# Optimization experiments

Hardware: AMD Instinct MI355X
Metric: run time of the kernel (lower is better)

The kernel has to match this reference:

```python
import jax, jax.numpy as jnp
import numpy as np

N_TX, N_USER, N_MERCH = 100000, 20000, 5000
E = 400000
F_IN, H, L = 32, 256, 2


def setup_inputs() -> dict:
    key = jax.random.key(0)
    ks = jax.random.split(key, 24)
    p = lambda k, s: 0.02 * jax.random.normal(k, s, dtype=jnp.float32)
    return {
        "x_tx": jax.random.normal(ks[0], (N_TX, F_IN), dtype=jnp.float32),
        "x_user": jax.random.normal(ks[1], (N_USER, H), dtype=jnp.float32),
        "x_merch": jax.random.normal(ks[2], (N_MERCH, H), dtype=jnp.float32),
        # input projection
        "Wp": p(ks[3], (F_IN, H)), "bp": jnp.zeros((H,), jnp.float32),
        # per-layer, per-edge-type SAGEConv params: lin_l (neighbor, with bias) and lin_r (root, no bias)
        "Wl": p(ks[4], (L, 4, H, H)), "bl": jnp.zeros((L, 4, H), jnp.float32),
        "Wr": p(ks[5], (L, 4, H, H)),
        # classifier head
        "Wc1": p(ks[6], (H, H // 2)), "bc1": jnp.zeros((H // 2,), jnp.float32),
        "Wc2": p(ks[7], (H // 2, 1)), "bc2": jnp.zeros((1,), jnp.float32),
        # revenue head
        "Wv1": p(ks[8], (H, H // 2)), "bv1": jnp.zeros((H // 2,), jnp.float32),
        "Wv2": p(ks[9], (H // 2, 1)), "bv2": jnp.zeros((1,), jnp.float32),
        # edge lists (src, dst) per relation
        "e_ut_src": jax.random.randint(ks[10], (E,), 0, N_USER, dtype=jnp.int32),
        "e_ut_dst": jax.random.randint(ks[11], (E,), 0, N_TX, dtype=jnp.int32),
        "e_tm_src": jax.random.randint(ks[12], (E,), 0, N_TX, dtype=jnp.int32),
        "e_tm_dst": jax.random.randint(ks[13], (E,), 0, N_MERCH, dtype=jnp.int32),
        "e_mt_src": jax.random.randint(ks[14], (E,), 0, N_MERCH, dtype=jnp.int32),
        "e_mt_dst": jax.random.randint(ks[15], (E,), 0, N_TX, dtype=jnp.int32),
        "e_tu_src": jax.random.randint(ks[16], (E,), 0, N_TX, dtype=jnp.int32),
        "e_tu_dst": jax.random.randint(ks[17], (E,), 0, N_USER, dtype=jnp.int32),
    }


def _seg_mean(x_src, src, dst, n_dst):
    # gather source features per edge, scatter-mean into destinations
    msg = x_src[src]                                        # [E, H]
    s = jax.ops.segment_sum(msg, dst, num_segments=n_dst)   # [n_dst, H]
    cnt = jax.ops.segment_sum(jnp.ones((dst.shape[0],), x_src.dtype), dst, num_segments=n_dst)
    return s / jnp.maximum(cnt, 1.0)[:, None]


def _sage(x_src, x_dst, src, dst, Wl, bl, Wr):
    # PyG SAGEConv: lin_l(mean_neighbors) + lin_r(x_dst)
    m = _seg_mean(x_src, src, dst, x_dst.shape[0])
    return m @ Wl + bl + x_dst @ Wr


def reference(x_tx, x_user, x_merch, Wp, bp, Wl, bl, Wr,
              Wc1, bc1, Wc2, bc2, Wv1, bv1, Wv2, bv2,
              e_ut_src, e_ut_dst, e_tm_src, e_tm_dst,
              e_mt_src, e_mt_dst, e_tu_src, e_tu_dst):
    xt = x_tx @ Wp + bp          # input_proj on 'transaction'
    xu, xm = x_user, x_merch     # already hidden_dim -> used as-is
    for l in range(L):
        t_from_u = _sage(xu, xt, e_ut_src, e_ut_dst, Wl[l, 0], bl[l, 0], Wr[l, 0])
        m_from_t = _sage(xt, xm, e_tm_src, e_tm_dst, Wl[l, 1], bl[l, 1], Wr[l, 1])
        t_from_m = _sage(xm, xt, e_mt_src, e_mt_dst, Wl[l, 2], bl[l, 2], Wr[l, 2])
        u_from_t = _sage(xt, xu, e_tu_src, e_tu_dst, Wl[l, 3], bl[l, 3], Wr[l, 3])
        # HeteroConv aggr='mean' over edge types per destination, then ReLU (dropout = identity in eval)
        xt = jax.nn.relu(0.5 * (t_from_u + t_from_m))
        xm = jax.nn.relu(m_from_t)
        xu = jax.nn.relu(u_from_t)
    fraud_logits = (jax.nn.relu(xt @ Wc1 + bc1) @ Wc2 + bc2)[:, 0]
    revenue_pred = (jax.nn.relu(xt @ Wv1 + bv1) @ Wv2 + bv2)[:, 0]
    return fraud_logits, revenue_pred
```

## Files before the change

kernel.cpp:

```cpp
#include <hip/hip_runtime.h>

#define NTX 100000
#define NUSER 20000
#define NMERCH 5000
#define HD 256
#define ROWPAD 128

using u16 = unsigned short;
typedef __attribute__((ext_vector_type(8))) short bf16x8;
typedef __attribute__((ext_vector_type(4))) float f32x4;

__device__ __forceinline__ u16 f2bf(float f){
  unsigned u = __float_as_uint(f);
  unsigned r = (u + 0x7FFFu + ((u >> 16) & 1u)) >> 16;
  return (u16)r;
}
__device__ __forceinline__ float bf2f(u16 b){
  return __uint_as_float(((unsigned)b) << 16);
}
__device__ __forceinline__ unsigned pk2(float a, float b){
  return (unsigned)f2bf(a) | ((unsigned)f2bf(b) << 16);
}

__device__ __forceinline__ void gather4(const u16* __restrict__ T, const int* __restrict__ ss,
    int j0, int j1, int lane, int c, float& o0, float& o1, float& o2, float& o3){
  float a0=0,a1=0,a2=0,a3=0, b0=0,b1=0,b2=0,b3=0;
  float c0=0,c1=0,c2=0,c3=0, d0=0,d1=0,d2=0,d3=0;
  for (int base = j0; base < j1; base += 64){
    int n = j1 - base; if (n > 64) n = 64;
    int idx = ss[base + (lane < n ? lane : 0)];
    for (int jj = 0; jj < n; jj += 4){
      int s0 = __shfl(idx, jj);
      int s1 = __shfl(idx, jj+1);
      int s2 = __shfl(idx, jj+2);
      int s3 = __shfl(idx, jj+3);
      ushort4 v0 = *(const ushort4*)(T + (size_t)s0*HD + c);
      ushort4 v1 = *(const ushort4*)(T + (size_t)s1*HD + c);
      ushort4 v2 = *(const ushort4*)(T + (size_t)s2*HD + c);
      ushort4 v3 = *(const ushort4*)(T + (size_t)s3*HD + c);
      a0 += bf2f(v0.x); a1 += bf2f(v0.y); a2 += bf2f(v0.z); a3 += bf2f(v0.w);
      if (jj+1 < n){ b0 += bf2f(v1.x); b1 += bf2f(v1.y); b2 += bf2f(v1.z); b3 += bf2f(v1.w); }
      if (jj+2 < n){ c0 += bf2f(v2.x); c1 += bf2f(v2.y); c2 += bf2f(v2.z); c3 += bf2f(v2.w); }
      if (jj+3 < n){ d0 += bf2f(v3.x); d1 += bf2f(v3.y); d2 += bf2f(v3.z); d3 += bf2f(v3.w); }
    }
  }
  o0 += (a0+b0)+(c0+d0); o1 += (a1+b1)+(c1+d1);
  o2 += (a2+b2)+(c2+d2); o3 += (a3+b3)+(c3+d3);
}

__device__ __forceinline__ int rel_n(int y){ return y==0?NTX: y==1?NMERCH: y==2?NTX:NUSER; }
__device__ __forceinline__ int rel_coff(int y){ return y==0?0: y==1?100000: y==2?105000:205000; }
__device__ __forceinline__ int rel_rpoff(int y){ return y==0?0: y==1?100001: y==2?105002:205003; }
__device__ __forceinline__ int rel_shift(int y){ return y==0?11: y==1?8: y==2?11:10; }
__device__ __forceinline__ int rel_np(int y){ return y==0?49: y==1?20: y==2?49:20; }
#define ECH 128
#define PSTW 72

__global__ __launch_bounds__(256) void csrA_kernel(const int* __restrict__ d0p, const int* __restrict__ d1p,
    const int* __restrict__ d2p, const int* __restrict__ d3p, int nE, int* __restrict__ PC){
  int y = blockIdx.y;
  const int* dst = y==0?d0p: y==1?d1p: y==2?d2p:d3p;
  int shift = rel_shift(y);
  __shared__ int cc[64];
  int t = threadIdx.x;
  if (t < 64) cc[t] = 0;
  __syncthreads();
  int CH = (nE + ECH - 1)/ECH;
  int e0 = blockIdx.x*CH, e1 = e0 + CH; if (e1 > nE) e1 = nE;
  for (int e = e0 + t*4; e < e1; e += 1024){
    int a = dst[e];
    int b = (e+1 < e1) ? dst[e+1] : -1;
    int c = (e+2 < e1) ? dst[e+2] : -1;
    int d = (e+3 < e1) ? dst[e+3] : -1;
    atomicAdd(&cc[a>>shift], 1);
    if (b >= 0) atomicAdd(&cc[b>>shift], 1);
    if (c >= 0) atomicAdd(&cc[c>>shift], 1);
    if (d >= 0) atomicAdd(&cc[d>>shift], 1);
  }
  __syncthreads();
  if (t < 64) PC[(((size_t)y*ECH + blockIdx.x)<<6) + t] = cc[t];
}

__global__ void csrB_kernel(int* __restrict__ PC, int* __restrict__ PST, int* __restrict__ RP, int nE){
  int y = blockIdx.y;
  int np = rel_np(y);
  int t = threadIdx.x;
  __shared__ int sh[64];
  int run = 0;
  if (t < np){
    for (int c = 0; c < ECH; ++c){
      size_t idx = (((size_t)y*ECH + c)<<6) + t;
      int v = PC[idx]; PC[idx] = run; run += v;
    }
  }
  sh[t] = run;
  __syncthreads();
  if (t == 0){
    int acc = 0;
    for (int i = 0; i < np; ++i){ int v = sh[i]; sh[i] = acc; acc += v; }
    PST[y*PSTW + np] = nE;
    RP[rel_rpoff(y) + rel_n(y)] = nE;
  }
  __syncthreads();
  if (t < np){
    int base = sh[t];
    PST[y*PSTW + t] = base;
    for (int c = 0; c < ECH; ++c){
      size_t idx = (((size_t)y*ECH + c)<<6) + t;
      PC[idx] += base;
    }
  }
}

__global__ __launch_bounds__(256) void csrC_kernel(
    const int* __restrict__ s0p, const int* __restrict__ d0p,
    const int* __restrict__ s1p, const int* __restrict__ d1p,
    const int* __restrict__ s2p, const int* __restrict__ d2p,
    const int* __restrict__ s3p, const int* __restrict__ d3p,
    const int* __restrict__ PC, int* __restrict__ EB, int nE){
  int y = blockIdx.y;
  const int* src = y==0?s0p: y==1?s1p: y==2?s2p:s3p;
  const int* dst = y==0?d0p: y==1?d1p: y==2?d2p:d3p;
  int shift = rel_shift(y);
  int mask = (1<<shift) - 1;
  __shared__ int cur[64];
  int t = threadIdx.x;
  if (t < 64) cur[t] = PC[(((size_t)y*ECH + blockIdx.x)<<6) + t];
  __syncthreads();
  int CH = (nE + ECH - 1)/ECH;
  int e0 = blockIdx.x*CH, e1 = e0 + CH; if (e1 > nE) e1 = nE;
  int* eb = EB + (size_t)y*nE;
  for (int e = e0 + t*4; e < e1; e += 1024){
    #pragma unroll
    for (int u = 0; u < 4; ++u){
      int ee = e + u;
      if (ee < e1){
        int d = dst[ee], s = src[ee];
        int pos = atomicAdd(&cur[d>>shift], 1);
        eb[pos] = ((d & mask) << 17) | s;
      }
    }
  }
}

__global__ __launch_bounds__(256) void csrD_kernel(const int* __restrict__ EB, const int* __restrict__ PST,
    int* __restrict__ RP, float* __restrict__ INV,
    int* __restrict__ ss0, int* __restrict__ ss1, int* __restrict__ ss2, int* __restrict__ ss3, int nE){
  int y = blockIdx.y;
  int np = rel_np(y);
  int part = blockIdx.x;
  if (part >= np) return;
  int shift = rel_shift(y);
  int n = rel_n(y);
  int gbase = part << shift;
  int len = n - gbase; int range = 1 << shift; if (len > range) len = range;
  __shared__ int cnt[2048];
  __shared__ int curs[2048];
  __shared__ int sh[256];
  int t = threadIdx.x;
  for (int i = t; i < len; i += 256) cnt[i] = 0;
  __syncthreads();
  const int* eb = EB + (size_t)y*nE;
  int j0 = PST[y*PSTW + part], j1 = PST[y*PSTW + part + 1];
  for (int j = j0 + t*4; j < j1; j += 1024){
    int a = eb[j];
    int b = (j+1 < j1) ? eb[j+1] : -1;
    int c = (j+2 < j1) ? eb[j+2] : -1;
    int d = (j+3 < j1) ? eb[j+3] : -1;
    atomicAdd(&cnt[a>>17], 1);
    if (b >= 0) atomicAdd(&cnt[b>>17], 1);
    if (c >= 0) atomicAdd(&cnt[c>>17], 1);
    if (d >= 0) atomicAdd(&cnt[d>>17], 1);
  }
  __syncthreads();
  int base8 = t*8;
  int vals[8]; int tsum = 0;
  #pragma unroll
  for (int u = 0; u < 8; ++u){
    int i = base8 + u;
    int v = (i < len) ? cnt[i] : 0;
    vals[u] = tsum; tsum += v;
  }
  sh[t] = tsum;
  __syncthreads();
  for (int o = 1; o < 256; o <<= 1){
    int v = (t >= o) ? sh[t-o] : 0;
    __syncthreads();
    sh[t] += v;
    __syncthreads();
  }
  int tbase = j0 + sh[t] - tsum;
  int rpo = rel_rpoff(y) + gbase;
  int ivo = rel_coff(y) + gbase;
  #pragma unroll
  for (int u = 0; u < 8; ++u){
    int i = base8 + u;
    if (i < len){
      int start = tbase + vals[u];
      curs[i] = start;
      RP[rpo + i] = start;
      INV[ivo + i] = 1.f/fmaxf((float)cnt[i], 1.f);
    }
  }
  __syncthreads();
  int* ss = y==0?ss0: y==1?ss1: y==2?ss2:ss3;
  for (int j = j0 + t*4; j < j1; j += 1024){
    #pragma unroll
    for (int u = 0; u < 4; ++u){
      int jj = j + u;
      if (jj < j1){
        int pk = eb[jj];
        int pos = atomicAdd(&curs[pk>>17], 1);
        ss[pos] = pk & 0x1FFFF;
      }
    }
  }
}

__global__ __launch_bounds__(256) void wprep_kernel(const float* __restrict__ Wl, const float* __restrict__ Wr,
    const float* __restrict__ Wp, const float* __restrict__ Wc1, const float* __restrict__ Wv1,
    const float* __restrict__ bc1, const float* __restrict__ bv1,
    u16* __restrict__ WTl, u16* __restrict__ WTr1, u16* __restrict__ WTr3, u16* __restrict__ WT02,
    u16* __restrict__ WTH, u16* __restrict__ WTp, float* __restrict__ bH){
  int y = blockIdx.y;
  int i = blockIdx.x*256 + threadIdx.x;
  if (y < 8){
    if (i < 65536){ int k=i>>8, n=i&255; WTl[(size_t)y*65536 + n*256 + k] = f2bf(Wl[(size_t)y*65536 + i]); }
  } else if (y < 10){
    int l = y-8;
    if (i < 65536){ int k=i>>8, n=i&255; WTr1[(size_t)l*65536 + n*256 + k] = f2bf(Wr[(size_t)(l*4+1)*65536 + i]); }
  } else if (y < 12){
    int l = y-10;
    if (i < 65536){ int k=i>>8, n=i&255; WTr3[(size_t)l*65536 + n*256 + k] = f2bf(Wr[(size_t)(l*4+3)*65536 + i]); }
  } else if (y < 14){
    int l = y-12;
    if (i < 65536){ int k=i>>8, n=i&255;
      WT02[(size_t)l*65536 + n*256 + k] = f2bf(Wr[(size_t)(l*4+0)*65536 + i] + Wr[(size_t)(l*4+2)*65536 + i]); }
  } else if (y == 14){
    if (i < 65536){ int k=i>>8, n=i&255;
      float v = (n < 128) ? Wc1[k*128 + n] : Wv1[k*128 + (n-128)];
      WTH[(size_t)n*256 + k] = f2bf(v); }
  } else {
    if (i < 8192){ int k=i>>8, n=i&255; WTp[(size_t)n*32 + k] = f2bf(Wp[i]); }
    if (i < 256) bH[i] = (i < 128) ? bc1[i] : bv1[i-128];
  }
}

__global__ __launch_bounds__(256) void cvt2_kernel(const float* __restrict__ xu,
    const float* __restrict__ xm, u16* __restrict__ XU, u16* __restrict__ XM){
  int y = blockIdx.y;
  const float* in = y==0?xu:xm;
  u16* out = y==0?XU:XM;
  int n4 = y==0?NUSER*HD/4:NMERCH*HD/4;
  int i = blockIdx.x*256 + threadIdx.x;
  if (i >= n4) return;
  float4 v = ((const float4*)in)[i];
  ushort4 o; o.x = f2bf(v.x); o.y = f2bf(v.y); o.z = f2bf(v.z); o.w = f2bf(v.w);
  ((ushort4*)out)[i] = o;
}

__global__ __launch_bounds__(256) void proj_gemm_kernel(const float* __restrict__ A, const u16* __restrict__ WT,
    const float* __restrict__ bias, u16* __restrict__ C, int M){
  __shared__ u16 As[128][40];
  __shared__ u16 Bs[128][40];
  int m0 = blockIdx.x * 128, n0 = blockIdx.y * 128;
  int t = threadIdx.x;
  int w = t >> 6, lane = t & 63;
  int wm = (w >> 1) << 6, wn = (w & 1) << 6;
  int lm = lane & 15;
  int lk = (lane >> 4) << 3;
  int sr = t >> 1, sc = (t & 1) << 4;
  float4 f0 = {0,0,0,0}, f1 = {0,0,0,0}, f2 = {0,0,0,0}, f3 = {0,0,0,0};
  if (m0 + sr < M){
    const float* ap = A + (size_t)(m0+sr)*32 + sc;
    f0 = *(const float4*)(ap+0); f1 = *(const float4*)(ap+4);
    f2 = *(const float4*)(ap+8); f3 = *(const float4*)(ap+12);
  }
  uint4 q0, q1;
  q0.x = pk2(f0.x,f0.y); q0.y = pk2(f0.z,f0.w); q0.z = pk2(f1.x,f1.y); q0.w = pk2(f1.z,f1.w);
  q1.x = pk2(f2.x,f2.y); q1.y = pk2(f2.z,f2.w); q1.z = pk2(f3.x,f3.y); q1.w = pk2(f3.z,f3.w);
  *(uint4*)&As[sr][sc] = q0;
  *(uint4*)&As[sr][sc+8] = q1;
  const u16* bp_ = WT + (size_t)(n0+sr)*32 + sc;
  *(uint4*)&Bs[sr][sc]   = *(const uint4*)(bp_);
  *(uint4*)&Bs[sr][sc+8] = *(const uint4*)(bp_ + 8);
  __syncthreads();
  bf16x8 af[4], bf[4];
  #pragma unroll
  for (int i = 0; i < 4; ++i) af[i] = *(const bf16x8*)&As[wm + i*16 + lm][lk];
  #pragma unroll
  for (int j = 0; j < 4; ++j) bf[j] = *(const bf16x8*)&Bs[wn + j*16 + lm][lk];
  f32x4 acc[4][4] = {};
  #pragma unroll
  for (int i = 0; i < 4; ++i)
    #pragma unroll
    for (int j = 0; j < 4; ++j)
      acc[i][j] = __builtin_amdgcn_mfma_f32_16x16x32_bf16(af[i], bf[j], acc[i][j], 0, 0, 0);
  int rsub = (lane >> 4) << 2;
  #pragma unroll
  for (int j = 0; j < 4; ++j){
    int col = n0 + wn + j*16 + lm;
    float bv = bias[col];
    #pragma unroll
    for (int i = 0; i < 4; ++i){
      int rbase = m0 + wm + i*16 + rsub;
      #pragma unroll
      for (int r = 0; r < 4; ++r){
        int row = rbase + r;
        if (row < M) C[(size_t)row*HD + col] = f2bf(acc[i][j][r] + bv);
      }
    }
  }
}

template<bool CBF, bool BIAS, bool RELU, bool ACCUM>
__global__ __launch_bounds__(256) void mfma_gemm_kernel(const u16* __restrict__ A, const u16* __restrict__ BT,
    const float* __restrict__ bias, const float* __restrict__ Cadd, void* __restrict__ Cp, int M, int K, int N){
  __shared__ u16 As[128][40];
  __shared__ u16 Bs[128][40];
  int m0 = blockIdx.x * 128, n0 = blockIdx.y * 128;
  int t = threadIdx.x;
  int w = t >> 6, lane = t & 63;
  int wm = (w >> 1) << 6, wn = (w & 1) << 6;
  int lm = lane & 15;
  int lk = (lane >> 4) << 3;
  f32x4 acc[4][4] = {};
  int sr0 = t >> 2,        sk0 = (t & 3) << 3;
  int sr1 = (t+256) >> 2,  sk1 = sk0;
  for (int k0 = 0; k0 < K; k0 += 32){
    uint4 a0 = *(const uint4*)(A  + (size_t)(m0+sr0)*K + k0 + sk0);
    uint4 a1 = *(const uint4*)(A  + (size_t)(m0+sr1)*K + k0 + sk1);
    uint4 b0 = *(const uint4*)(BT + (size_t)(n0+sr0)*K + k0 + sk0);
    uint4 b1 = *(const uint4*)(BT + (size_t)(n0+sr1)*K + k0 + sk1);
    *(uint4*)&As[sr0][sk0] = a0;
    *(uint4*)&As[sr1][sk1] = a1;
    *(uint4*)&Bs[sr0][sk0] = b0;
    *(uint4*)&Bs[sr1][sk1] = b1;
    __syncthreads();
    bf16x8 af[4], bf[4];
    #pragma unroll
    for (int i = 0; i < 4; ++i) af[i] = *(const bf16x8*)&As[wm + i*16 + lm][lk];
    #pragma unroll
    for (int j = 0; j < 4; ++j) bf[j] = *(const bf16x8*)&Bs[wn + j*16 + lm][lk];
    #pragma unroll
    for (int i = 0; i < 4; ++i)
      #pragma unroll
      for (int j = 0; j < 4; ++j)
        acc[i][j] = __builtin_amdgcn_mfma_f32_16x16x32_bf16(af[i], bf[j], acc[i][j], 0, 0, 0);
    __syncthreads();
  }
  int rsub = (lane >> 4) << 2;
  #pragma unroll
  for (int j = 0; j < 4; ++j){
    int col = n0 + wn + j*16 + lm;
    float bv = 0.f;
    if constexpr (BIAS) bv = bias[col];
    #pragma unroll
    for (int i = 0; i < 4; ++i){
      int rbase = m0 + wm + i*16 + rsub;
      #pragma unroll
      for (int r = 0; r < 4; ++r){
        int row = rbase + r;
        if (row < M){
          float v = acc[i][j][r] + bv;
          if constexpr (ACCUM) v += Cadd[(size_t)row*N + col];
          if constexpr (RELU) v = fmaxf(v, 0.f);
          if constexpr (CBF) ((u16*)Cp)[(size_t)row*N + col] = f2bf(v);
          else               ((float*)Cp)[(size_t)row*N + col] = v;
        }
      }
    }
  }
}

__global__ __launch_bounds__(256) void pair_gemm_kernel(
    const u16* __restrict__ A0, const u16* __restrict__ W0, u16* __restrict__ C0, int M0,
    const u16* __restrict__ A1, const u16* __restrict__ W1, u16* __restrict__ C1, int M1){
  int z = blockIdx.z;
  const u16* A = z ? A1 : A0;
  const u16* WT = z ? W1 : W0;
  u16* C = z ? C1 : C0;
  int M = z ? M1 : M0;
  int m0 = blockIdx.x * 128, n0 = blockIdx.y * 128;
  if (m0 >= M) return;
  __shared__ u16 As[128][40];
  __shared__ u16 Bs[128][40];
  int t = threadIdx.x;
  int w = t >> 6, lane = t & 63;
  int wm = (w >> 1) << 6, wn = (w & 1) << 6;
  int lm = lane & 15;
  int lk = (lane >> 4) << 3;
  f32x4 acc[4][4] = {};
  int sr0 = t >> 2,        sk0 = (t & 3) << 3;
  int sr1 = (t+256) >> 2,  sk1 = sk0;
  for (int k0 = 0; k0 < 256; k0 += 32){
    uint4 a0 = *(const uint4*)(A  + (size_t)(m0+sr0)*256 + k0 + sk0);
    uint4 a1 = *(const uint4*)(A  + (size_t)(m0+sr1)*256 + k0 + sk1);
    uint4 b0 = *(const uint4*)(WT + (size_t)(n0+sr0)*256 + k0 + sk0);
    uint4 b1 = *(const uint4*)(WT + (size_t)(n0+sr1)*256 + k0 + sk1);
    *(uint4*)&As[sr0][sk0] = a0;
    *(uint4*)&As[sr1][sk1] = a1;
    *(uint4*)&Bs[sr0][sk0] = b0;
    *(uint4*)&Bs[sr1][sk1] = b1;
    __syncthreads();
    bf16x8 af[4], bf[4];
    #pragma unroll
    for (int i = 0; i < 4; ++i) af[i] = *(const bf16x8*)&As[wm + i*16 + lm][lk];
    #pragma unroll
    for (int j = 0; j < 4; ++j) bf[j] = *(const bf16x8*)&Bs[wn + j*16 + lm][lk];
    #pragma unroll
    for (int i = 0; i < 4; ++i)
      #pragma unroll
      for (int j = 0; j < 4; ++j)
        acc[i][j] = __builtin_amdgcn_mfma_f32_16x16x32_bf16(af[i], bf[j], acc[i][j], 0, 0, 0);
    __syncthreads();
  }
  int rsub = (lane >> 4) << 2;
  #pragma unroll
  for (int j = 0; j < 4; ++j){
    int col = n0 + wn + j*16 + lm;
    #pragma unroll
    for (int i = 0; i < 4; ++i){
      int rbase = m0 + wm + i*16 + rsub;
      #pragma unroll
      for (int r = 0; r < 4; ++r){
        int row = rbase + r;
        if (row < M) C[(size_t)row*256 + col] = f2bf(acc[i][j][r]);
      }
    }
  }
}

__global__ __launch_bounds__(256) void pair_gemm2_kernel(
    const u16* __restrict__ G0, const u16* __restrict__ X0, const u16* __restrict__ Wa0, const u16* __restrict__ Wb0,
    const float* __restrict__ b0, u16* __restrict__ C0, int M0,
    const u16* __restrict__ G1, const u16* __restrict__ X1, const u16* __restrict__ Wa1, const u16* __restrict__ Wb1,
    const float* __restrict__ b1, u16* __restrict__ C1, int M1){
  int z = blockIdx.z;
  const u16* G  = z ? G1 : G0;
  const u16* X  = z ? X1 : X0;
  const u16* Wa = z ? Wa1 : Wa0;
  const u16* Wb = z ? Wb1 : Wb0;
  const float* bias = z ? b1 : b0;
  u16* C = z ? C1 : C0;
  int M = z ? M1 : M0;
  int m0 = blockIdx.x * 128, n0 = blockIdx.y * 128;
  if (m0 >= M) return;
  __shared__ u16 As[128][40];
  __shared__ u16 Bs[128][40];
  int t = threadIdx.x;
  int w = t >> 6, lane = t & 63;
  int wm = (w >> 1) << 6, wn = (w & 1) << 6;
  int lm = lane & 15;
  int lk = (lane >> 4) << 3;
  f32x4 acc[4][4] = {};
  int sr0 = t >> 2,        sk0 = (t & 3) << 3;
  int sr1 = (t+256) >> 2,  sk1 = sk0;
  for (int k0 = 0; k0 < 512; k0 += 32){
    const u16* A  = (k0 < 256) ? G : X;
    const u16* WT = (k0 < 256) ? Wa : Wb;
    int kk = k0 & 255;
    uint4 a0 = *(const uint4*)(A  + (size_t)(m0+sr0)*256 + kk + sk0);
    uint4 a1 = *(const uint4*)(A  + (size_t)(m0+sr1)*256 + kk + sk1);
    uint4 b0_ = *(const uint4*)(WT + (size_t)(n0+sr0)*256 + kk + sk0);
    uint4 b1_ = *(const uint4*)(WT + (size_t)(n0+sr1)*256 + kk + sk1);
    *(uint4*)&As[sr0][sk0] = a0;
    *(uint4*)&As[sr1][sk1] = a1;
    *(uint4*)&Bs[sr0][sk0] = b0_;
    *(uint4*)&Bs[sr1][sk1] = b1_;
    __syncthreads();
    bf16x8 af[4], bf[4];
    #pragma unroll
    for (int i = 0; i < 4; ++i) af[i] = *(const bf16x8*)&As[wm + i*16 + lm][lk];
    #pragma unroll
    for (int j = 0; j < 4; ++j) bf[j] = *(const bf16x8*)&Bs[wn + j*16 + lm][lk];
    #pragma unroll
    for (int i = 0; i < 4; ++i)
      #pragma unroll
      for (int j = 0; j < 4; ++j)
        acc[i][j] = __builtin_amdgcn_mfma_f32_16x16x32_bf16(af[i], bf[j], acc[i][j], 0, 0, 0);
    __syncthreads();
  }
  int rsub = (lane >> 4) << 2;
  #pragma unroll
  for (int j = 0; j < 4; ++j){
    int col = n0 + wn + j*16 + lm;
    float bv = bias[col];
    #pragma unroll
    for (int i = 0; i < 4; ++i){
      int rbase = m0 + wm + i*16 + rsub;
      #pragma unroll
      for (int r = 0; r < 4; ++r){
        int row = rbase + r;
        if (row < M) C[(size_t)row*256 + col] = f2bf(fmaxf(acc[i][j][r] + bv, 0.f));
      }
    }
  }
}

__global__ __launch_bounds__(256) void gather_pair_kernel(const u16* __restrict__ XT,
    const int* __restrict__ rp0, const int* __restrict__ ss0, const float* __restrict__ inv0,
    u16* __restrict__ out0, int M0,
    const int* __restrict__ rp1, const int* __restrict__ ss1, const float* __restrict__ inv1,
    u16* __restrict__ out1, int M1){
  int y = blockIdx.y;
  const int* rp = y ? rp1 : rp0;
  const int* ss = y ? ss1 : ss0;
  const float* inv = y ? inv1 : inv0;
  u16* out = y ? out1 : out0;
  int M = y ? M1 : M0;
  int d = blockIdx.x*4 + (threadIdx.x >> 6);
  if (d >= M) return;
  int lane = threadIdx.x & 63;
  int c = lane << 2;
  float o0=0,o1=0,o2=0,o3=0;
  gather4(XT, ss, rp[d], rp[d+1], lane, c, o0, o1, o2, o3);
  float sc = inv[d];
  ushort4 o; o.x = f2bf(o0*sc); o.y = f2bf(o1*sc); o.z = f2bf(o2*sc); o.w = f2bf(o3*sc);
  *(ushort4*)(out + (size_t)d*HD + c) = o;
}

__global__ __launch_bounds__(256) void fused_tx_kernel(const u16* __restrict__ ACCb,
    const u16* __restrict__ Tu, const u16* __restrict__ Tm,
    const int* __restrict__ rpu, const int* __restrict__ ssu, const float* __restrict__ invu,
    const int* __restrict__ rpm, const int* __restrict__ ssm, const float* __restrict__ invm,
    const float* __restrict__ b0, const float* __restrict__ b2, u16* __restrict__ XT, int M){
  int d = blockIdx.x*4 + (threadIdx.x >> 6);
  if (d >= M) return;
  int lane = threadIdx.x & 63;
  int c = lane << 2;
  ushort4 av = *(const ushort4*)(ACCb + (size_t)d*HD + c);
  float r0 = bf2f(av.x), r1 = bf2f(av.y), r2 = bf2f(av.z), r3 = bf2f(av.w);
  {
    float s0=0,s1=0,s2=0,s3=0;
    gather4(Tu, ssu, rpu[d], rpu[d+1], lane, c, s0, s1, s2, s3);
    float sc = invu[d];
    r0 += s0*sc; r1 += s1*sc; r2 += s2*sc; r3 += s3*sc;
  }
  {
    float s0=0,s1=0,s2=0,s3=0;
    gather4(Tm, ssm, rpm[d], rpm[d+1], lane, c, s0, s1, s2, s3);
    float sc = invm[d];
    r0 += s0*sc; r1 += s1*sc; r2 += s2*sc; r3 += s3*sc;
  }
  float4 bb0 = *(const float4*)(b0 + c);
  float4 bb2 = *(const float4*)(b2 + c);
  ushort4 o;
  o.x = f2bf(fmaxf(0.5f*(r0 + bb0.x + bb2.x), 0.f));
  o.y = f2bf(fmaxf(0.5f*(r1 + bb0.y + bb2.y), 0.f));
  o.z = f2bf(fmaxf(0.5f*(r2 + bb0.z + bb2.z), 0.f));
  o.w = f2bf(fmaxf(0.5f*(r3 + bb0.w + bb2.w), 0.f));
  *(ushort4*)(XT + (size_t)d*HD + c) = o;
}

__global__ __launch_bounds__(256) void head_kernel(const u16* __restrict__ Hm, const float* __restrict__ Wc2,
    const float* __restrict__ bc2, const float* __restrict__ Wv2, const float* __restrict__ bv2,
    float* __restrict__ out, int M){
  int row = blockIdx.x*4 + (threadIdx.x >> 6);
  if (row >= M) return;
  int lane = threadIdx.x & 63;
  const u16* h = Hm + (size_t)row*256;
  float s1 = bf2f(h[lane])*Wc2[lane] + bf2f(h[lane+64])*Wc2[lane+64];
  float s2 = bf2f(h[128+lane])*Wv2[lane] + bf2f(h[192+lane])*Wv2[lane+64];
  #pragma unroll
  for (int off = 32; off > 0; off >>= 1){
    s1 += __shfl_down(s1, off);
    s2 += __shfl_down(s2, off);
  }
  if (lane == 0){ out[row] = s1 + bc2[0]; out[M+row] = s2 + bv2[0]; }
}

extern "C" void kernel_launch(void* const* d_in, const int* in_sizes, int n_in,
                              void* d_out, int out_size, void* d_ws, size_t ws_size,
                              hipStream_t stream){
  const float* x_tx   = (const float*)d_in[0];
  const float* x_user = (const float*)d_in[1];
  const float* x_merch= (const float*)d_in[2];
  const float* Wp  = (const float*)d_in[3];
  const float* bp  = (const float*)d_in[4];
  const float* Wl  = (const float*)d_in[5];
  const float* bl  = (const float*)d_in[6];
  const float* Wr  = (const float*)d_in[7];
  const float* Wc1 = (const float*)d_in[8];
  const float* bc1 = (const float*)d_in[9];
  const float* Wc2 = (const float*)d_in[10];
  const float* bc2 = (const float*)d_in[11];
  const float* Wv1 = (const float*)d_in[12];
  const float* bv1 = (const float*)d_in[13];
  const float* Wv2 = (const float*)d_in[14];
  const float* bv2 = (const float*)d_in[15];
  const int* e_ut_s = (const int*)d_in[16];
  const int* e_ut_d = (const int*)d_in[17];
  const int* e_tm_s = (const int*)d_in[18];
  const int* e_tm_d = (const int*)d_in[19];
  const int* e_mt_s = (const int*)d_in[20];
  const int* e_mt_d = (const int*)d_in[21];
  const int* e_tu_s = (const int*)d_in[22];
  const int* e_tu_d = (const int*)d_in[23];
  float* out = (float*)d_out;
  const int NE = in_sizes[16];

  char* p = (char*)d_ws;
  auto take = [&](size_t bytes)->char*{ char* r = p; p += (bytes + 255) & ~(size_t)255; return r; };
  u16*   XT    = (u16*)  take((size_t)(NTX+ROWPAD)*HD*2);
  u16*   ACCb  = (u16*)  take((size_t)(NTX+ROWPAD)*HD*2);
  u16*   Tu    = (u16*)  take((size_t)NUSER*HD*2);
  u16*   Tm    = (u16*)  take((size_t)NMERCH*HD*2);
  u16*   AGGU  = (u16*)  take((size_t)(NUSER+ROWPAD)*HD*2);
  u16*   AGGM  = (u16*)  take((size_t)(NMERCH+ROWPAD)*HD*2);
  u16*   XU0   = (u16*)  take((size_t)(NUSER+ROWPAD)*HD*2);
  u16*   XU1   = (u16*)  take((size_t)(NUSER+ROWPAD)*HD*2);
  u16*   XM0   = (u16*)  take((size_t)(NMERCH+ROWPAD)*HD*2);
  u16*   XM1   = (u16*)  take((size_t)(NMERCH+ROWPAD)*HD*2);
  float* INV   = (float*)take((size_t)225000*4);
  int*   RP    = (int*)  take((size_t)225008*4);
  int*   SS_ut = (int*)  take((size_t)NE*4);
  int*   SS_tm = (int*)  take((size_t)NE*4);
  int*   SS_mt = (int*)  take((size_t)NE*4);
  int*   SS_tu = (int*)  take((size_t)NE*4);
  int*   PC    = (int*)  take((size_t)4*ECH*64*4);
  int*   PST   = (int*)  take((size_t)4*PSTW*4);
  int*   EB    = (int*)  take((size_t)4*NE*4);
  u16*   WTp   = (u16*)  take((size_t)32*256*2);
  u16*   WTl   = (u16*)  take((size_t)8*65536*2);
  u16*   WTr1  = (u16*)  take((size_t)2*65536*2);
  u16*   WTr3  = (u16*)  take((size_t)2*65536*2);
  u16*   WT02  = (u16*)  take((size_t)2*65536*2);
  u16*   WTH   = (u16*)  take((size_t)65536*2);
  float* bH    = (float*)take((size_t)256*4);

  float* inv_ut = INV,  *inv_tm = INV+100000, *inv_mt = INV+105000, *inv_tu = INV+205000;
  int*   rp_ut  = RP,   *rp_tm  = RP+100001,  *rp_mt  = RP+105002,  *rp_tu  = RP+205003;

  csrA_kernel<<<dim3(ECH,4),256,0,stream>>>(e_ut_d, e_tm_d, e_mt_d, e_tu_d, NE, PC);
  csrB_kernel<<<dim3(1,4),64,0,stream>>>(PC, PST, RP, NE);
  csrC_kernel<<<dim3(ECH,4),256,0,stream>>>(e_ut_s, e_ut_d, e_tm_s, e_tm_d, e_mt_s, e_mt_d,
      e_tu_s, e_tu_d, PC, EB, NE);
  csrD_kernel<<<dim3(49,4),256,0,stream>>>(EB, PST, RP, INV, SS_ut, SS_tm, SS_mt, SS_tu, NE);

  wprep_kernel<<<dim3(256,16),256,0,stream>>>(Wl, Wr, Wp, Wc1, Wv1, bc1, bv1,
      WTl, WTr1, WTr3, WT02, WTH, WTp, bH);

  cvt2_kernel<<<dim3(5000,2),256,0,stream>>>(x_user, x_merch, XU0, XM0);
  proj_gemm_kernel<<<dim3(782,2),256,0,stream>>>(x_tx, WTp, bp, XT, NTX);

  u16* xu_cur = XU0; u16* xu_nxt = XU1;
  u16* xm_cur = XM0; u16* xm_nxt = XM1;

  for (int l = 0; l < 2; ++l){
    const float* bl_l = bl + (size_t)l*4*256;
    u16* WTl_l = WTl + (size_t)l*4*65536;

    gather_pair_kernel<<<dim3(5000,2),256,0,stream>>>(XT,
        rp_tm, SS_tm, inv_tm, AGGM, NMERCH,
        rp_tu, SS_tu, inv_tu, AGGU, NUSER);

    pair_gemm_kernel<<<dim3(157,2,2),256,0,stream>>>(
        xu_cur, WTl_l + 0*65536, Tu, NUSER,
        xm_cur, WTl_l + 2*65536, Tm, NMERCH);

    mfma_gemm_kernel<true,false,false,false><<<dim3(782,2),256,0,stream>>>(
        XT, WT02 + (size_t)l*65536, nullptr, nullptr, ACCb, NTX, 256, 256);
    fused_tx_kernel<<<(NTX+3)/4,256,0,stream>>>(ACCb, Tu, Tm,
        rp_ut, SS_ut, inv_ut, rp_mt, SS_mt, inv_mt,
        bl_l + 0*256, bl_l + 2*256, XT, NTX);

    pair_gemm2_kernel<<<dim3(157,2,2),256,0,stream>>>(
        AGGU, xu_cur, WTl_l + 3*65536, WTr3 + (size_t)l*65536, bl_l + 3*256, xu_nxt, NUSER,
        AGGM, xm_cur, WTl_l + 1*65536, WTr1 + (size_t)l*65536, bl_l + 1*256, xm_nxt, NMERCH);

    { u16* tmp = xu_cur; xu_cur = xu_nxt; xu_nxt = tmp; }
    { u16* tmp = xm_cur; xm_cur = xm_nxt; xm_nxt = tmp; }
  }

  mfma_gemm_kernel<true,true,true,false><<<dim3(782,2),256,0,stream>>>(
      XT, WTH, bH, nullptr, ACCb, NTX, 256, 256);
  head_kernel<<<(NTX+3)/4,256,0,stream>>>(ACCb, Wc2, bc2, Wv2, bv2, out, NTX);
}
```

Before: 581.0 us.

## Fuse root GEMM with transaction gather epilogue and fuse head GEMM with reduction

The transaction root GEMM now stages its bf16 tile in LDS and, in the same kernel, gathers user and merchant neighbor features for each row. It then adds biases, applies ReLU and writes the new transaction features into a ping-pong buffer, so the ACCb round trip and a separate launch go away. The head GEMM likewise does bias, ReLU and the dot with Wc2/Wv2 in registers, reducing with shuffles and LDS atomics, so the hidden matrix is never written. The cost is that the per-row gather inside GEMM blocks now runs with two columns per lane and one wave per 32 rows serially, which may cut gather parallelism and occupancy.

```diff
diff --git a/kernel.cpp b/kernel.cpp
--- a/kernel.cpp
+++ b/kernel.cpp
@@ -46,6 +46,30 @@
   }
   o0 += (a0+b0)+(c0+d0); o1 += (a1+b1)+(c1+d1);
   o2 += (a2+b2)+(c2+d2); o3 += (a3+b3)+(c3+d3);
+}
+
+__device__ __forceinline__ void gather2(const u16* __restrict__ T, const int* __restrict__ ss,
+    int j0, int j1, int lane, int cg, float& o0, float& o1){
+  float a0=0,a1=0,b0=0,b1=0,c0=0,c1=0,d0=0,d1=0;
+  for (int base = j0; base < j1; base += 64){
+    int n = j1 - base; if (n > 64) n = 64;
+    int idx = ss[base + (lane < n ? lane : 0)];
+    for (int jj = 0; jj < n; jj += 4){
+      int s0 = __shfl(idx, jj);
+      int s1 = __shfl(idx, jj+1);
+      int s2 = __shfl(idx, jj+2);
+      int s3 = __shfl(idx, jj+3);
+      unsigned v0 = *(const unsigned*)(T + (size_t)s0*HD + cg);
+      unsigned v1 = (jj+1 < n) ? *(const unsigned*)(T + (size_t)s1*HD + cg) : 0u;
+      unsigned v2 = (jj+2 < n) ? *(const unsigned*)(T + (size_t)s2*HD + cg) : 0u;
+      unsigned v3 = (jj+3 < n) ? *(const unsigned*)(T + (size_t)s3*HD + cg) : 0u;
+      a0 += bf2f((u16)(v0 & 0xffff)); a1 += bf2f((u16)(v0 >> 16));
+      b0 += bf2f((u16)(v1 & 0xffff)); b1 += bf2f((u16)(v1 >> 16));
+      c0 += bf2f((u16)(v2 & 0xffff)); c1 += bf2f((u16)(v2 >> 16));
+      d0 += bf2f((u16)(v3 & 0xffff)); d1 += bf2f((u16)(v3 >> 16));
+    }
+  }
+  o0 += (a0+b0)+(c0+d0); o1 += (a1+b1)+(c1+d1);
 }
 
 __device__ __forceinline__ int rel_n(int y){ return y==0?NTX: y==1?NMERCH: y==2?NTX:NUSER; }
@@ -313,11 +337,14 @@
   }
 }
 
-template<bool CBF, bool BIAS, bool RELU, bool ACCUM>
-__global__ __launch_bounds__(256) void mfma_gemm_kernel(const u16* __restrict__ A, const u16* __restrict__ BT,
-    const float* __restrict__ bias, const float* __restrict__ Cadd, void* __restrict__ Cp, int M, int K, int N){
-  __shared__ u16 As[128][40];
-  __shared__ u16 Bs[128][40];
+__global__ __launch_bounds__(256) void fused_root_tx_kernel(const u16* __restrict__ A, const u16* __restrict__ BT,
+    const u16* __restrict__ Tu, const u16* __restrict__ Tm,
+    const int* __restrict__ rpu, const int* __restrict__ ssu, const float* __restrict__ invu,
+    const int* __restrict__ rpm, const int* __restrict__ ssm, const float* __restrict__ invm,
+    const float* __restrict__ b0, const float* __restrict__ b2, u16* __restrict__ XTo, int M){
+  __shared__ u16 lds[17408];
+  u16* As = lds;
+  u16* Bs = lds + 5120;
   int m0 = blockIdx.x * 128, n0 = blockIdx.y * 128;
   int t = threadIdx.x;
   int w = t >> 6, lane = t & 63;
@@ -325,23 +352,23 @@
   int lm = lane & 15;
   int lk = (lane >> 4) << 3;
   f32x4 acc[4][4] = {};
-  int sr0 = t >> 2,        sk0 = (t & 3) << 3;
-  int sr1 = (t+256) >> 2,  sk1 = sk0;
-  for (int k0 = 0; k0 < K; k0 += 32){
-    uint4 a0 = *(const uint4*)(A  + (size_t)(m0+sr0)*K + k0 + sk0);
-    uint4 a1 = *(const uint4*)(A  + (size_t)(m0+sr1)*K + k0 + sk1);
-    uint4 b0 = *(const uint4*)(BT + (size_t)(n0+sr0)*K + k0 + sk0);
-    uint4 b1 = *(const uint4*)(BT + (size_t)(n0+sr1)*K + k0 + sk1);
-    *(uint4*)&As[sr0][sk0] = a0;
-    *(uint4*)&As[sr1][sk1] = a1;
-    *(uint4*)&Bs[sr0][sk0] = b0;
-    *(uint4*)&Bs[sr1][sk1] = b1;
+  int sr0 = t >> 2, sk0 = (t & 3) << 3;
+  int sr1 = sr0 + 64;
+  for (int k0 = 0; k0 < 256; k0 += 32){
+    uint4 a0 = *(const uint4*)(A  + (size_t)(m0+sr0)*256 + k0 + sk0);
+    uint4 a1 = *(const uint4*)(A  + (size_t)(m0+sr1)*256 + k0 + sk0);
+    uint4 b0_ = *(const uint4*)(BT + (size_t)(n0+sr0)*256 + k0 + sk0);
+    uint4 b1_ = *(const uint4*)(BT + (size_t)(n0+sr1)*256 + k0 + sk0);
+    *(uint4*)&As[sr0*40 + sk0] = a0;
+    *(uint4*)&As[sr1*40 + sk0] = a1;
+    *(uint4*)&Bs[sr0*40 + sk0] = b0_;
+    *(uint4*)&Bs[sr1*40 + sk0] = b1_;
     __syncthreads();
     bf16x8 af[4], bf[4];
     #pragma unroll
-    for (int i = 0; i < 4; ++i) af[i] = *(const bf16x8*)&As[wm + i*16 + lm][lk];
-    #pragma unroll
-    for (int j = 0; j < 4; ++j) bf[j] = *(const bf16x8*)&Bs[wn + j*16 + lm][lk];
+    for (int i = 0; i < 4; ++i) af[i] = *(const bf16x8*)&As[(wm + i*16 + lm)*40 + lk];
+    #pragma unroll
+    for (int j = 0; j < 4; ++j) bf[j] = *(const bf16x8*)&Bs[(wn + j*16 + lm)*40 + lk];
     #pragma unroll
     for (int i = 0; i < 4; ++i)
       #pragma unroll
@@ -352,24 +379,31 @@
   int rsub = (lane >> 4) << 2;
   #pragma unroll
   for (int j = 0; j < 4; ++j){
-    int col = n0 + wn + j*16 + lm;
-    float bv = 0.f;
-    if constexpr (BIAS) bv = bias[col];
+    int cl = wn + j*16 + lm;
     #pragma unroll
     for (int i = 0; i < 4; ++i){
-      int rbase = m0 + wm + i*16 + rsub;
-      #pragma unroll
-      for (int r = 0; r < 4; ++r){
-        int row = rbase + r;
-        if (row < M){
-          float v = acc[i][j][r] + bv;
-          if constexpr (ACCUM) v += Cadd[(size_t)row*N + col];
-          if constexpr (RELU) v = fmaxf(v, 0.f);
-          if constexpr (CBF) ((u16*)Cp)[(size_t)row*N + col] = f2bf(v);
-          else               ((float*)Cp)[(size_t)row*N + col] = v;
-        }
-      }
-    }
+      int rb = wm + i*16 + rsub;
+      #pragma unroll
+      for (int r = 0; r < 4; ++r) lds[(rb + r)*136 + cl] = f2bf(acc[i][j][r]);
+    }
+  }
+  __syncthreads();
+  int cg = n0 + lane*2;
+  float2 bb0 = *(const float2*)(b0 + cg);
+  float2 bb2 = *(const float2*)(b2 + cg);
+  for (int rr = 0; rr < 32; ++rr){
+    int rl = w*32 + rr;
+    int row = m0 + rl;
+    if (row >= M) break;
+    float s0 = bf2f(lds[rl*136 + lane*2]);
+    float s1 = bf2f(lds[rl*136 + lane*2 + 1]);
+    float u0 = 0.f, u1 = 0.f, v0 = 0.f, v1 = 0.f;
+    gather2(Tu, ssu, rpu[row], rpu[row+1], lane, cg, u0, u1);
+    gather2(Tm, ssm, rpm[row], rpm[row+1], lane, cg, v0, v1);
+    float iu = invu[row], im = invm[row];
+    float r0 = fmaxf(0.5f*(s0 + u0*iu + v0*im + bb0.x + bb2.x), 0.f);
+    float r1 = fmaxf(0.5f*(s1 + u1*iu + v1*im + bb0.y + bb2.y), 0.f);
+    *(unsigned*)(XTo + (size_t)row*HD + cg) = pk2(r0, r1);
   }
 }
 
@@ -391,17 +425,17 @@
   int lm = lane & 15;
   int lk = (lane >> 4) << 3;
   f32x4 acc[4][4] = {};
-  int sr0 = t >> 2,        sk0 = (t & 3) << 3;
-  int sr1 = (t+256) >> 2,  sk1 = sk0;
+  int sr0 = t >> 2, sk0 = (t & 3) << 3;
+  int sr1 = sr0 + 64;
   for (int k0 = 0; k0 < 256; k0 += 32){
     uint4 a0 = *(const uint4*)(A  + (size_t)(m0+sr0)*256 + k0 + sk0);
-    uint4 a1 = *(const uint4*)(A  + (size_t)(m0+sr1)*256 + k0 + sk1);
+    uint4 a1 = *(const uint4*)(A  + (size_t)(m0+sr1)*256 + k0 + sk0);
     uint4 b0 = *(const uint4*)(WT + (size_t)(n0+sr0)*256 + k0 + sk0);
-    uint4 b1 = *(const uint4*)(WT + (size_t)(n0+sr1)*256 + k0 + sk1);
+    uint4 b1 = *(const uint4*)(WT + (size_t)(n0+sr1)*256 + k0 + sk0);
     *(uint4*)&As[sr0][sk0] = a0;
-    *(uint4*)&As[sr1][sk1] = a1;
+    *(uint4*)&As[sr1][sk0] = a1;
     *(uint4*)&Bs[sr0][sk0] = b0;
-    *(uint4*)&Bs[sr1][sk1] = b1;
+    *(uint4*)&Bs[sr1][sk0] = b1;
     __syncthreads();
     bf16x8 af[4], bf[4];
     #pragma unroll
@@ -454,20 +488,20 @@
   int lm = lane & 15;
   int lk = (lane >> 4) << 3;
   f32x4 acc[4][4] = {};
-  int sr0 = t >> 2,        sk0 = (t & 3) << 3;
-  int sr1 = (t+256) >> 2,  sk1 = sk0;
+  int sr0 = t >> 2, sk0 = (t & 3) << 3;
+  int sr1 = sr0 + 64;
   for (int k0 = 0; k0 < 512; k0 += 32){
     const u16* A  = (k0 < 256) ? G : X;
     const u16* WT = (k0 < 256) ? Wa : Wb;
     int kk = k0 & 255;
     uint4 a0 = *(const uint4*)(A  + (size_t)(m0+sr0)*256 + kk + sk0);
-    uint4 a1 = *(const uint4*)(A  + (size_t)(m0+sr1)*256 + kk + sk1);
+    uint4 a1 = *(const uint4*)(A  + (size_t)(m0+sr1)*256 + kk + sk0);
     uint4 b0_ = *(const uint4*)(WT + (size_t)(n0+sr0)*256 + kk + sk0);
-    uint4 b1_ = *(const uint4*)(WT + (size_t)(n0+sr1)*256 + kk + sk1);
+    uint4 b1_ = *(const uint4*)(WT + (size_t)(n0+sr1)*256 + kk + sk0);
     *(uint4*)&As[sr0][sk0] = a0;
-    *(uint4*)&As[sr1][sk1] = a1;
+    *(uint4*)&As[sr1][sk0] = a1;
     *(uint4*)&Bs[sr0][sk0] = b0_;
-    *(uint4*)&Bs[sr1][sk1] = b1_;
+    *(uint4*)&Bs[sr1][sk0] = b1_;
     __syncthreads();
     bf16x8 af[4], bf[4];
     #pragma unroll
@@ -520,54 +554,71 @@
   *(ushort4*)(out + (size_t)d*HD + c) = o;
 }
 
-__global__ __launch_bounds__(256) void fused_tx_kernel(const u16* __restrict__ ACCb,
-    const u16* __restrict__ Tu, const u16* __restrict__ Tm,
-    const int* __restrict__ rpu, const int* __restrict__ ssu, const float* __restrict__ invu,
-    const int* __restrict__ rpm, const int* __restrict__ ssm, const float* __restrict__ invm,
-    const float* __restrict__ b0, const float* __restrict__ b2, u16* __restrict__ XT, int M){
-  int d = blockIdx.x*4 + (threadIdx.x >> 6);
-  if (d >= M) return;
-  int lane = threadIdx.x & 63;
-  int c = lane << 2;
-  ushort4 av = *(const ushort4*)(ACCb + (size_t)d*HD + c);
-  float r0 = bf2f(av.x), r1 = bf2f(av.y), r2 = bf2f(av.z), r3 = bf2f(av.w);
-  {
-    float s0=0,s1=0,s2=0,s3=0;
-    gather4(Tu, ssu, rpu[d], rpu[d+1], lane, c, s0, s1, s2, s3);
-    float sc = invu[d];
-    r0 += s0*sc; r1 += s1*sc; r2 += s2*sc; r3 += s3*sc;
-  }
-  {
-    float s0=0,s1=0,s2=0,s3=0;
-    gather4(Tm, ssm, rpm[d], rpm[d+1], lane, c, s0, s1, s2, s3);
-    float sc = invm[d];
-    r0 += s0*sc; r1 += s1*sc; r2 += s2*sc; r3 += s3*sc;
-  }
-  float4 bb0 = *(const float4*)(b0 + c);
-  float4 bb2 = *(const float4*)(b2 + c);
-  ushort4 o;
-  o.x = f2bf(fmaxf(0.5f*(r0 + bb0.x + bb2.x), 0.f));
-  o.y = f2bf(fmaxf(0.5f*(r1 + bb0.y + bb2.y), 0.f));
-  o.z = f2bf(fmaxf(0.5f*(r2 + bb0.z + bb2.z), 0.f));
-  o.w = f2bf(fmaxf(0.5f*(r3 + bb0.w + bb2.w), 0.f));
-  *(ushort4*)(XT + (size_t)d*HD + c) = o;
-}
-
-__global__ __launch_bounds__(256) void head_kernel(const u16* __restrict__ Hm, const float* __restrict__ Wc2,
-    const float* __restrict__ bc2, const float* __restrict__ Wv2, const float* __restrict__ bv2,
-    float* __restrict__ out, int M){
-  int row = blockIdx.x*4 + (threadIdx.x >> 6);
-  if (row >= M) return;
-  int lane = threadIdx.x & 63;
-  const u16* h = Hm + (size_t)row*256;
-  float s1 = bf2f(h[lane])*Wc2[lane] + bf2f(h[lane+64])*Wc2[lane+64];
-  float s2 = bf2f(h[128+lane])*Wv2[lane] + bf2f(h[192+lane])*Wv2[lane+64];
-  #pragma unroll
-  for (int off = 32; off > 0; off >>= 1){
-    s1 += __shfl_down(s1, off);
-    s2 += __shfl_down(s2, off);
-  }
-  if (lane == 0){ out[row] = s1 + bc2[0]; out[M+row] = s2 + bv2[0]; }
+__global__ __launch_bounds__(256) void fused_head_kernel(const u16* __restrict__ A, const u16* __restrict__ BT,
+    const float* __restrict__ bias, const float* __restrict__ Wc2, const float* __restrict__ bc2,
+    const float* __restrict__ Wv2, const float* __restrict__ bv2, float* __restrict__ out, int M){
+  __shared__ u16 As[128][40];
+  __shared__ u16 Bs[128][40];
+  __shared__ float hpart[128];
+  int m0 = blockIdx.x * 128, n0 = blockIdx.y * 128;
+  int t = threadIdx.x;
+  int w = t >> 6, lane = t & 63;
+  int wm = (w >> 1) << 6, wn = (w & 1) << 6;
+  int lm = lane & 15;
+  int lk = (lane >> 4) << 3;
+  if (t < 128) hpart[t] = 0.f;
+  f32x4 acc[4][4] = {};
+  int sr0 = t >> 2, sk0 = (t & 3) << 3;
+  int sr1 = sr0 + 64;
+  for (int k0 = 0; k0 < 256; k0 += 32){
+    uint4 a0 = *(const uint4*)(A  + (size_t)(m0+sr0)*256 + k0 + sk0);
+    uint4 a1 = *(const uint4*)(A  + (size_t)(m0+sr1)*256 + k0 + sk0);
+    uint4 b0 = *(const uint4*)(BT + (size_t)(n0+sr0)*256 + k0 + sk0);
+    uint4 b1 = *(const uint4*)(BT + (size_t)(n0+sr1)*256 + k0 + sk0);
+    *(uint4*)&As[sr0][sk0] = a0;
+    *(uint4*)&As[sr1][sk0] = a1;
+    *(uint4*)&Bs[sr0][sk0] = b0;
+    *(uint4*)&Bs[sr1][sk0] = b1;
+    __syncthreads();
+    bf16x8 af[4], bf[4];
+    #pragma unroll
+    for (int i = 0; i < 4; ++i) af[i] = *(const bf16x8*)&As[wm + i*16 + lm][lk];
+    #pragma unroll
+    for (int j = 0; j < 4; ++j) bf[j] = *(const bf16x8*)&Bs[wn + j*16 + lm][lk];
+    #pragma unroll
+    for (int i = 0; i < 4; ++i)
+      #pragma unroll
+      for (int j = 0; j < 4; ++j)
+        acc[i][j] = __builtin_amdgcn_mfma_f32_16x16x32_bf16(af[i], bf[j], acc[i][j], 0, 0, 0);
+    __syncthreads();
+  }
+  const float* w2 = blockIdx.y ? Wv2 : Wc2;
+  float badd = blockIdx.y ? bv2[0] : bc2[0];
+  size_t outoff = blockIdx.y ? (size_t)M : 0;
+  int rsub = (lane >> 4) << 2;
+  float w2v[4], bv[4];
+  #pragma unroll
+  for (int j = 0; j < 4; ++j){
+    w2v[j] = w2[wn + j*16 + lm];
+    bv[j]  = bias[n0 + wn + j*16 + lm];
+  }
+  #pragma unroll
+  for (int i = 0; i < 4; ++i){
+    #pragma unroll
+    for (int r = 0; r < 4; ++r){
+      float p = 0.f;
+      #pragma unroll
+      for (int j = 0; j < 4; ++j) p += fmaxf(acc[i][j][r] + bv[j], 0.f) * w2v[j];
+      p += __shfl_xor(p, 1); p += __shfl_xor(p, 2);
+      p += __shfl_xor(p, 4); p += __shfl_xor(p, 8);
+      if (lm == 0) atomicAdd(&hpart[wm + i*16 + rsub + r], p);
+    }
+  }
+  __syncthreads();
+  if (t < 128){
+    int row = m0 + t;
+    if (row < M) out[outoff + row] = hpart[t] + badd;
+  }
 }
 
 extern "C" void kernel_launch(void* const* d_in, const int* in_sizes, int n_in,
@@ -603,7 +654,7 @@
   char* p = (char*)d_ws;
   auto take = [&](size_t bytes)->char*{ char* r = p; p += (bytes + 255) & ~(size_t)255; return r; };
   u16*   XT    = (u16*)  take((size_t)(NTX+ROWPAD)*HD*2);
-  u16*   ACCb  = (u16*)  take((size_t)(NTX+ROWPAD)*HD*2);
+  u16*   XTB   = (u16*)  take((size_t)(NTX+ROWPAD)*HD*2);
   u16*   Tu    = (u16*)  take((size_t)NUSER*HD*2);
   u16*   Tm    = (u16*)  take((size_t)NMERCH*HD*2);
   u16*   AGGU  = (u16*)  take((size_t)(NUSER+ROWPAD)*HD*2);
@@ -644,6 +695,7 @@
   cvt2_kernel<<<dim3(5000,2),256,0,stream>>>(x_user, x_merch, XU0, XM0);
   proj_gemm_kernel<<<dim3(782,2),256,0,stream>>>(x_tx, WTp, bp, XT, NTX);
 
+  u16* xt_cur = XT;  u16* xt_nxt = XTB;
   u16* xu_cur = XU0; u16* xu_nxt = XU1;
   u16* xm_cur = XM0; u16* xm_nxt = XM1;
 
@@ -651,7 +703,7 @@
     const float* bl_l = bl + (size_t)l*4*256;
     u16* WTl_l = WTl + (size_t)l*4*65536;
 
-    gather_pair_kernel<<<dim3(5000,2),256,0,stream>>>(XT,
+    gather_pair_kernel<<<dim3(5000,2),256,0,stream>>>(xt_cur,
         rp_tm, SS_tm, inv_tm, AGGM, NMERCH,
         rp_tu, SS_tu, inv_tu, AGGU, NUSER);
 
@@ -659,21 +711,19 @@
         xu_cur, WTl_l + 0*65536, Tu, NUSER,
         xm_cur, WTl_l + 2*65536, Tm, NMERCH);
 
-    mfma_gemm_kernel<true,false,false,false><<<dim3(782,2),256,0,stream>>>(
-        XT, WT02 + (size_t)l*65536, nullptr, nullptr, ACCb, NTX, 256, 256);
-    fused_tx_kernel<<<(NTX+3)/4,256,0,stream>>>(ACCb, Tu, Tm,
+    fused_root_tx_kernel<<<dim3(782,2),256,0,stream>>>(
+        xt_cur, WT02 + (size_t)l*65536, Tu, Tm,
         rp_ut, SS_ut, inv_ut, rp_mt, SS_mt, inv_mt,
-        bl_l + 0*256, bl_l + 2*256, XT, NTX);
+        bl_l + 0*256, bl_l + 2*256, xt_nxt, NTX);
 
     pair_gemm2_kernel<<<dim3(157,2,2),256,0,stream>>>(
         AGGU, xu_cur, WTl_l + 3*65536, WTr3 + (size_t)l*65536, bl_l + 3*256, xu_nxt, NUSER,
         AGGM, xm_cur, WTl_l + 1*65536, WTr1 + (size_t)l*65536, bl_l + 1*256, xm_nxt, NMERCH);
 
+    { u16* tmp = xt_cur; xt_cur = xt_nxt; xt_nxt = tmp; }
     { u16* tmp = xu_cur; xu_cur = xu_nxt; xu_nxt = tmp; }
     { u16* tmp = xm_cur; xm_cur = xm_nxt; xm_nxt = tmp; }
   }
 
-  mfma_gemm_kernel<true,true,true,false><<<dim3(782,2),256,0,stream>>>(
-      XT, WTH, bH, nullptr, ACCb, NTX, 256, 256);
-  head_kernel<<<(NTX+3)/4,256,0,stream>>>(ACCb, Wc2, bc2, Wv2, bv2, out, NTX);
-}
+  fused_head_kernel<<<dim3(782,2),256,0,stream>>>(xt_cur, WTH, bH, Wc2, bc2, Wv2, bv2, out, NTX);
+}
```

Measured after the change: 731.4 us. +25.9%, slower.
